# Performance work log

Measured on AMD Instinct MI355X. Metric: run time of the kernel, lower is better.

## Reference

```python
import jax, jax.numpy as jnp
import numpy as np

BN_EPS = 1e-5

def setup_inputs() -> dict:
    key = jax.random.key(0)
    ks = jax.random.split(key, 12)
    B = 32768
    x = jax.random.normal(ks[0], (B, 1, 28, 28), dtype=jnp.float32)
    conv_w = jax.random.normal(ks[1], (5, 1, 6, 6), dtype=jnp.float32) * 0.1
    conv_b = jax.random.normal(ks[2], (5,), dtype=jnp.float32) * 0.1
    bn2_gamma = jnp.ones((5,), jnp.float32) + jax.random.normal(ks[3], (5,), jnp.float32) * 0.05
    bn2_beta = jax.random.normal(ks[4], (5,), jnp.float32) * 0.05
    bn2_mean = jax.random.normal(ks[5], (5,), jnp.float32) * 0.1
    bn2_var = jax.random.uniform(ks[6], (5,), jnp.float32, 0.5, 1.5)
    fc_w = jax.random.normal(ks[7], (10, 125), dtype=jnp.float32) * 0.1
    fc_b = jax.random.normal(ks[8], (10,), dtype=jnp.float32) * 0.1
    bn1_gamma = jnp.ones((10,), jnp.float32) + jax.random.normal(ks[9], (10,), jnp.float32) * 0.05
    bn1_beta = jax.random.normal(ks[10], (10,), jnp.float32) * 0.05
    bn1_mean = jax.random.normal(ks[11], (10,), jnp.float32) * 0.1
    bn1_var = jnp.ones((10,), jnp.float32)
    return {"x": x, "conv_w": conv_w, "conv_b": conv_b,
            "bn2_gamma": bn2_gamma, "bn2_beta": bn2_beta, "bn2_mean": bn2_mean, "bn2_var": bn2_var,
            "fc_w": fc_w, "fc_b": fc_b,
            "bn1_gamma": bn1_gamma, "bn1_beta": bn1_beta, "bn1_mean": bn1_mean, "bn1_var": bn1_var}

def _sign(t):
    # torch Binarize = tensor.sign()
    return jnp.sign(t)

def reference(x, conv_w, conv_b, bn2_gamma, bn2_beta, bn2_mean, bn2_var,
              fc_w, fc_b, bn1_gamma, bn1_beta, bn1_mean, bn1_var):
    # BinarizeConv2d: binarize both input (C_in=1 != 3) and weight
    xb = _sign(x)
    wb = _sign(conv_w)
    y = jax.lax.conv_general_dilated(
        xb, wb, window_strides=(6, 6), padding=((2, 2), (2, 2)),
        dimension_numbers=("NCHW", "OIHW", "NCHW"))  # [B,5,5,5]
    y = y + conv_b[None, :, None, None]
    # BatchNorm2d (eval-mode running stats)
    y = (y - bn2_mean[None, :, None, None]) * (bn2_gamma / jnp.sqrt(bn2_var + BN_EPS))[None, :, None, None] + bn2_beta[None, :, None, None]
    # Hardtanh
    y = jnp.clip(y, -1.0, 1.0)
    # flatten to [B, 125]
    y = y.reshape(-1, 125)
    # BinarizeLinear: binarize input (125 != 784) and weight
    z = _sign(y) @ _sign(fc_w).T + fc_b
    # BatchNorm1d
    z = (z - bn1_mean) * (bn1_gamma / jnp.sqrt(bn1_var + BN_EPS)) + bn1_beta
    return jax.nn.log_softmax(z, axis=1)
```

## Files before the change

### kernel.cpp

```cpp
#include <hip/hip_runtime.h>
#include <cstdint>

#define BLK 256
#define SPB 8
#define RS  9
#define SS  (30*RS)
#define HDR 16
#define XS_INTS (HDR + SPB*SS)
#define YS_W 33

#if defined(__has_builtin)
# if __has_builtin(__builtin_amdgcn_sdot4)
#  define HAVE_SDOT4 1
# endif
#endif

__device__ __forceinline__ int dot4i8(int a, int b, int c) {
#ifdef HAVE_SDOT4
    return __builtin_amdgcn_sdot4(a, b, c, false);
#else
    int r = c;
    r += (((int)(a << 24)) >> 24) * (((int)(b << 24)) >> 24);
    r += (((int)(a << 16)) >> 24) * (((int)(b << 16)) >> 24);
    r += (((int)(a <<  8)) >> 24) * (((int)(b <<  8)) >> 24);
    r += (a >> 24) * (b >> 24);
    return r;
#endif
}

__device__ __forceinline__ int pack_sign4(float4 v) {
    int b0 = (v.x > 0.f) - (v.x < 0.f);
    int b1 = (v.y > 0.f) - (v.y < 0.f);
    int b2 = (v.z > 0.f) - (v.z < 0.f);
    int b3 = (v.w > 0.f) - (v.w < 0.f);
    return (b0 & 0xFF) | ((b1 & 0xFF) << 8) | ((b2 & 0xFF) << 16) | (b3 << 24);
}

__global__ void bnn_setup(const float* __restrict__ conv_w, const float* __restrict__ conv_b,
                          const float* __restrict__ bn2_g, const float* __restrict__ bn2_b,
                          const float* __restrict__ bn2_m, const float* __restrict__ bn2_v,
                          const float* __restrict__ fc_w,  const float* __restrict__ fc_b,
                          const float* __restrict__ bn1_g, const float* __restrict__ bn1_b,
                          const float* __restrict__ bn1_m, const float* __restrict__ bn1_v,
                          int* __restrict__ ws)
{
    const int tid = threadIdx.x;
    if (tid < 30) {
        int c = tid / 6, kr = tid - c * 6;
        const float* wp = conv_w + c * 36 + kr * 6;
        uint32_t a = 0, b = 0;
        #pragma unroll
        for (int k = 0; k < 4; k++) { int s = (wp[k]   > 0.f) - (wp[k]   < 0.f); a |= (uint32_t)(s & 0xFF) << (8 * k); }
        #pragma unroll
        for (int k = 0; k < 2; k++) { int s = (wp[4+k] > 0.f) - (wp[4+k] < 0.f); b |= (uint32_t)(s & 0xFF) << (8 * k); }
        ws[tid] = (int)a;
        ws[30 + tid] = (int)b;
    }
    for (int i = tid; i < 330; i += 64) {
        int o = i / 33, w = i - o * 33;
        uint32_t m = 0;
        #pragma unroll
        for (int k = 0; k < 4; k++) {
            int kk = w * 4 + k;
            if (kk < 125) { float f = fc_w[o * 125 + kk]; int s = (f > 0.f) - (f < 0.f); m |= (uint32_t)(s & 0xFF) << (8 * k); }
        }
        ws[60 + i] = (int)m;
    }
    if (tid < 5) {
        float sc = bn2_g[tid] / sqrtf(bn2_v[tid] + 1e-5f);
        ((float*)ws)[390 + tid] = sc;
        ((float*)ws)[395 + tid] = (conv_b[tid] - bn2_m[tid]) * sc + bn2_b[tid];
    }
    if (tid >= 32 && tid < 42) {
        int o = tid - 32;
        float sc = bn1_g[o] / sqrtf(bn1_v[o] + 1e-5f);
        ((float*)ws)[400 + o] = sc;
        ((float*)ws)[410 + o] = (fc_b[o] - bn1_m[o]) * sc + bn1_b[o];
    }
}

__global__ __launch_bounds__(BLK, 4)
void bnn_main(const float* __restrict__ x, const int* __restrict__ ws,
              float* __restrict__ out)
{
    __shared__ int   xsi[XS_INTS];
    __shared__ int   ysi[SPB * YS_W];
    __shared__ int   wsS[420];
    __shared__ float zf[SPB * 10];

    const int tid = threadIdx.x;
    const int blk = blockIdx.x;

    const float4* xg = (const float4*)x + (size_t)blk * (SPB * 196);
    float4 v[6]; float4 v6;
    #pragma unroll
    for (int k = 0; k < 6; k++) v[k] = xg[tid + k * BLK];
    const bool has7 = tid < (SPB * 196 - 6 * BLK);
    if (has7) v6 = xg[tid + 6 * BLK];

    for (int i = tid; i < 420; i += BLK) wsS[i] = ws[i];

    for (int i = tid; i < HDR + SPB * 74; i += BLK) {
        int idx;
        if (i < HDR) idx = i;
        else {
            int j = i - HDR, s = j / 74, k = j - s * 74;
            idx = HDR + s * SS + (k < 18 ? k : (2 + (k - 18) / 2) * RS + 7 + ((k - 18) & 1));
        }
        xsi[idx] = 0;
    }
    for (int i = tid; i < SPB * YS_W; i += BLK) ysi[i] = 0;

    #pragma unroll
    for (int k = 0; k < 6; k++) {
        int idx = tid + k * BLK;
        int s = idx / 196, rem = idx - s * 196;
        int r = rem / 7,   cq  = rem - r * 7;
        xsi[HDR + s * SS + (r + 2) * RS + cq] = pack_sign4(v[k]);
    }
    if (has7) {
        int idx = tid + 6 * BLK;
        int s = idx / 196, rem = idx - s * 196;
        int r = rem / 7,   cq  = rem - r * 7;
        xsi[HDR + s * SS + (r + 2) * RS + cq] = pack_sign4(v6);
    }
    __syncthreads();

    if (tid < 250) {
        const int c  = tid / 50;
        const int jb = tid - c * 50;
        int w0r[6], w1r[6];
        #pragma unroll
        for (int kr = 0; kr < 6; kr++) { w0r[kr] = wsS[c * 6 + kr]; w1r[kr] = wsS[30 + c * 6 + kr]; }
        const float sc = __int_as_float(wsS[390 + c]);
        const float bi = __int_as_float(wsS[395 + c]);
        #pragma unroll
        for (int t = 0; t < (SPB * 25) / 50; t++) {
            int j  = jb + 50 * t;
            int s  = j / 25, pos = j - s * 25;
            int oh = pos / 5, ow  = pos - oh * 5;
            int boff = 64 + s * (SS * 4) + oh * (6 * RS * 4) + ow * 6 - 2;
            int wi = boff >> 2;
            int sh = (boff & 3) * 8;
            int acc = 0;
            #pragma unroll
            for (int kr = 0; kr < 6; kr++) {
                uint32_t a0 = (uint32_t)xsi[wi + kr * RS];
                uint32_t a1 = (uint32_t)xsi[wi + kr * RS + 1];
                uint64_t vv = (((uint64_t)a1) << 32) | a0;
                vv >>= sh;
                acc = dot4i8((int)(uint32_t)vv,         w0r[kr], acc);
                acc = dot4i8((int)(uint32_t)(vv >> 32), w1r[kr], acc);
            }
            float yv = (float)acc * sc + bi;
            ((signed char*)ysi)[s * (YS_W * 4) + c * 25 + pos] =
                (signed char)((yv > 0.f) - (yv < 0.f));
        }
    }
    __syncthreads();

    if (tid < SPB * 10) {
        int s = tid / 10, o = tid - s * 10;
        int acc = 0;
        #pragma unroll
        for (int w = 0; w < 32; w++)
            acc = dot4i8(ysi[s * YS_W + w], wsS[60 + o * 33 + w], acc);
        zf[tid] = (float)acc * __int_as_float(wsS[400 + o]) + __int_as_float(wsS[410 + o]);
    }
    __syncthreads();

    if (tid < SPB) {
        float vv[10], mx = -1e30f;
        #pragma unroll
        for (int o = 0; o < 10; o++) { vv[o] = zf[tid * 10 + o]; mx = fmaxf(mx, vv[o]); }
        float l = 0.f;
        #pragma unroll
        for (int o = 0; o < 10; o++) l += __expf(vv[o] - mx);
        float lse = mx + __logf(l);
        #pragma unroll
        for (int o = 0; o < 10; o++) zf[tid * 10 + o] = vv[o] - lse;
    }
    __syncthreads();

    for (int i = tid; i < SPB * 10; i += BLK)
        out[(size_t)blk * (SPB * 10) + i] = zf[i];
}

extern "C" void kernel_launch(void* const* d_in, const int* in_sizes, int n_in,
                              void* d_out, int out_size, void* d_ws, size_t ws_size,
                              hipStream_t stream)
{
    const float* xp     = (const float*)d_in[0];
    const float* conv_w = (const float*)d_in[1];
    const float* conv_b = (const float*)d_in[2];
    const float* bn2_g  = (const float*)d_in[3];
    const float* bn2_b  = (const float*)d_in[4];
    const float* bn2_m  = (const float*)d_in[5];
    const float* bn2_v  = (const float*)d_in[6];
    const float* fc_w   = (const float*)d_in[7];
    const float* fc_b   = (const float*)d_in[8];
    const float* bn1_g  = (const float*)d_in[9];
    const float* bn1_b  = (const float*)d_in[10];
    const float* bn1_m  = (const float*)d_in[11];
    const float* bn1_v  = (const float*)d_in[12];
    float* outp = (float*)d_out;
    int*   ws   = (int*)d_ws;

    const int B = in_sizes[0] / 784;
    const int grid = B / SPB;

    bnn_setup<<<1, 64, 0, stream>>>(conv_w, conv_b, bn2_g, bn2_b, bn2_m, bn2_v,
                                    fc_w, fc_b, bn1_g, bn1_b, bn1_m, bn1_v, ws);
    bnn_main<<<grid, BLK, 0, stream>>>(xp, ws, outp);
}
```

Baseline: 179.8 us.

## Fuse weight setup into main kernel, double samples per block, restructure conv

Removes the separate setup kernel launch by having every block binarize conv/fc weights and fold the BN constants into shared memory. Doubles samples per block to 16 and rewrites the conv so each thread computes all 5 output channels for one spatial position. The 6x6 window is split into a 4-column part and a packed 2-column part, which cuts the dot-product count and reuses the loaded window across channels. In exchange every block redundantly reads and binarizes the small weight tensors, and register use rises from the 45 weight values held per thread.

```diff
diff --git a/kernel.cpp b/kernel.cpp
--- a/kernel.cpp
+++ b/kernel.cpp
@@ -2,12 +2,24 @@
 #include <cstdint>
 
 #define BLK 256
-#define SPB 8
+#define SPB 16
 #define RS  9
-#define SS  (30*RS)
+#define ROWS 30
+#define SS  (ROWS*RS)
 #define HDR 16
 #define XS_INTS (HDR + SPB*SS)
 #define YS_W 33
+#define NQ  ((SPB*196)/BLK)
+#define NREM (SPB*196 - NQ*BLK)
+
+#define W0_OFF  0
+#define W1P_OFF 30
+#define FC_OFF  45
+#define CSC_OFF 375
+#define CBI_OFF 380
+#define FSC_OFF 385
+#define FBI_OFF 395
+#define WS_TOT  405
 
 #if defined(__has_builtin)
 # if __has_builtin(__builtin_amdgcn_sdot4)
@@ -36,69 +48,72 @@
     return (b0 & 0xFF) | ((b1 & 0xFF) << 8) | ((b2 & 0xFF) << 16) | (b3 << 24);
 }
 
-__global__ void bnn_setup(const float* __restrict__ conv_w, const float* __restrict__ conv_b,
-                          const float* __restrict__ bn2_g, const float* __restrict__ bn2_b,
-                          const float* __restrict__ bn2_m, const float* __restrict__ bn2_v,
-                          const float* __restrict__ fc_w,  const float* __restrict__ fc_b,
-                          const float* __restrict__ bn1_g, const float* __restrict__ bn1_b,
-                          const float* __restrict__ bn1_m, const float* __restrict__ bn1_v,
-                          int* __restrict__ ws)
+__device__ __forceinline__ int sign8(float f) {
+    return (f > 0.f) - (f < 0.f);
+}
+
+__global__ __launch_bounds__(BLK, 4)
+void bnn_fused(const float* __restrict__ x,
+               const float* __restrict__ conv_w, const float* __restrict__ conv_b,
+               const float* __restrict__ bn2_g,  const float* __restrict__ bn2_b,
+               const float* __restrict__ bn2_m,  const float* __restrict__ bn2_v,
+               const float* __restrict__ fc_w,   const float* __restrict__ fc_b,
+               const float* __restrict__ bn1_g,  const float* __restrict__ bn1_b,
+               const float* __restrict__ bn1_m,  const float* __restrict__ bn1_v,
+               float* __restrict__ out)
 {
+    __shared__ int   xsi[XS_INTS];
+    __shared__ int   ysi[SPB * YS_W];
+    __shared__ int   wsS[WS_TOT];
+    __shared__ float zf[SPB * 10];
+
     const int tid = threadIdx.x;
+    const int blk = blockIdx.x;
+
+    const float4* xg = (const float4*)x + (size_t)blk * (SPB * 196);
+    float4 v[NQ]; float4 vr;
+    #pragma unroll
+    for (int k = 0; k < NQ; k++) v[k] = xg[tid + k * BLK];
+    const bool has = tid < NREM;
+    if (has) vr = xg[tid + NQ * BLK];
+
     if (tid < 30) {
         int c = tid / 6, kr = tid - c * 6;
         const float* wp = conv_w + c * 36 + kr * 6;
-        uint32_t a = 0, b = 0;
-        #pragma unroll
-        for (int k = 0; k < 4; k++) { int s = (wp[k]   > 0.f) - (wp[k]   < 0.f); a |= (uint32_t)(s & 0xFF) << (8 * k); }
-        #pragma unroll
-        for (int k = 0; k < 2; k++) { int s = (wp[4+k] > 0.f) - (wp[4+k] < 0.f); b |= (uint32_t)(s & 0xFF) << (8 * k); }
-        ws[tid] = (int)a;
-        ws[30 + tid] = (int)b;
-    }
-    for (int i = tid; i < 330; i += 64) {
+        uint32_t a = 0;
+        #pragma unroll
+        for (int k = 0; k < 4; k++) a |= (uint32_t)(sign8(wp[k]) & 0xFF) << (8 * k);
+        wsS[W0_OFF + tid] = (int)a;
+    } else if (tid >= 32 && tid < 47) {
+        int i = tid - 32, c = i / 3, p = i - c * 3;
+        const float* wp = conv_w + c * 36;
+        uint32_t a = 0;
+        a |= (uint32_t)(sign8(wp[(2*p)*6 + 4]) & 0xFF);
+        a |= (uint32_t)(sign8(wp[(2*p)*6 + 5]) & 0xFF) << 8;
+        a |= (uint32_t)(sign8(wp[(2*p+1)*6 + 4]) & 0xFF) << 16;
+        a |= (uint32_t)(sign8(wp[(2*p+1)*6 + 5]) & 0xFF) << 24;
+        wsS[W1P_OFF + i] = (int)a;
+    } else if (tid >= 48 && tid < 53) {
+        int c = tid - 48;
+        float sc = bn2_g[c] / sqrtf(bn2_v[c] + 1e-5f);
+        wsS[CSC_OFF + c] = __float_as_int(sc);
+        wsS[CBI_OFF + c] = __float_as_int((conv_b[c] - bn2_m[c]) * sc + bn2_b[c]);
+    } else if (tid >= 64 && tid < 74) {
+        int o = tid - 64;
+        float sc = bn1_g[o] / sqrtf(bn1_v[o] + 1e-5f);
+        wsS[FSC_OFF + o] = __float_as_int(sc);
+        wsS[FBI_OFF + o] = __float_as_int((fc_b[o] - bn1_m[o]) * sc + bn1_b[o]);
+    }
+    for (int i = tid; i < 330; i += BLK) {
         int o = i / 33, w = i - o * 33;
         uint32_t m = 0;
         #pragma unroll
         for (int k = 0; k < 4; k++) {
             int kk = w * 4 + k;
-            if (kk < 125) { float f = fc_w[o * 125 + kk]; int s = (f > 0.f) - (f < 0.f); m |= (uint32_t)(s & 0xFF) << (8 * k); }
-        }
-        ws[60 + i] = (int)m;
-    }
-    if (tid < 5) {
-        float sc = bn2_g[tid] / sqrtf(bn2_v[tid] + 1e-5f);
-        ((float*)ws)[390 + tid] = sc;
-        ((float*)ws)[395 + tid] = (conv_b[tid] - bn2_m[tid]) * sc + bn2_b[tid];
-    }
-    if (tid >= 32 && tid < 42) {
-        int o = tid - 32;
-        float sc = bn1_g[o] / sqrtf(bn1_v[o] + 1e-5f);
-        ((float*)ws)[400 + o] = sc;
-        ((float*)ws)[410 + o] = (fc_b[o] - bn1_m[o]) * sc + bn1_b[o];
-    }
-}
-
-__global__ __launch_bounds__(BLK, 4)
-void bnn_main(const float* __restrict__ x, const int* __restrict__ ws,
-              float* __restrict__ out)
-{
-    __shared__ int   xsi[XS_INTS];
-    __shared__ int   ysi[SPB * YS_W];
-    __shared__ int   wsS[420];
-    __shared__ float zf[SPB * 10];
-
-    const int tid = threadIdx.x;
-    const int blk = blockIdx.x;
-
-    const float4* xg = (const float4*)x + (size_t)blk * (SPB * 196);
-    float4 v[6]; float4 v6;
-    #pragma unroll
-    for (int k = 0; k < 6; k++) v[k] = xg[tid + k * BLK];
-    const bool has7 = tid < (SPB * 196 - 6 * BLK);
-    if (has7) v6 = xg[tid + 6 * BLK];
-
-    for (int i = tid; i < 420; i += BLK) wsS[i] = ws[i];
+            if (kk < 125) m |= (uint32_t)(sign8(fc_w[o * 125 + kk]) & 0xFF) << (8 * k);
+        }
+        wsS[FC_OFF + i] = (int)m;
+    }
 
     for (int i = tid; i < HDR + SPB * 74; i += BLK) {
         int idx;
@@ -112,49 +127,63 @@
     for (int i = tid; i < SPB * YS_W; i += BLK) ysi[i] = 0;
 
     #pragma unroll
-    for (int k = 0; k < 6; k++) {
+    for (int k = 0; k < NQ; k++) {
         int idx = tid + k * BLK;
         int s = idx / 196, rem = idx - s * 196;
         int r = rem / 7,   cq  = rem - r * 7;
         xsi[HDR + s * SS + (r + 2) * RS + cq] = pack_sign4(v[k]);
     }
-    if (has7) {
-        int idx = tid + 6 * BLK;
+    if (has) {
+        int idx = tid + NQ * BLK;
         int s = idx / 196, rem = idx - s * 196;
         int r = rem / 7,   cq  = rem - r * 7;
-        xsi[HDR + s * SS + (r + 2) * RS + cq] = pack_sign4(v6);
-    }
-    __syncthreads();
-
-    if (tid < 250) {
-        const int c  = tid / 50;
-        const int jb = tid - c * 50;
-        int w0r[6], w1r[6];
-        #pragma unroll
-        for (int kr = 0; kr < 6; kr++) { w0r[kr] = wsS[c * 6 + kr]; w1r[kr] = wsS[30 + c * 6 + kr]; }
-        const float sc = __int_as_float(wsS[390 + c]);
-        const float bi = __int_as_float(wsS[395 + c]);
-        #pragma unroll
-        for (int t = 0; t < (SPB * 25) / 50; t++) {
-            int j  = jb + 50 * t;
-            int s  = j / 25, pos = j - s * 25;
-            int oh = pos / 5, ow  = pos - oh * 5;
-            int boff = 64 + s * (SS * 4) + oh * (6 * RS * 4) + ow * 6 - 2;
-            int wi = boff >> 2;
-            int sh = (boff & 3) * 8;
-            int acc = 0;
-            #pragma unroll
-            for (int kr = 0; kr < 6; kr++) {
-                uint32_t a0 = (uint32_t)xsi[wi + kr * RS];
-                uint32_t a1 = (uint32_t)xsi[wi + kr * RS + 1];
-                uint64_t vv = (((uint64_t)a1) << 32) | a0;
-                vv >>= sh;
-                acc = dot4i8((int)(uint32_t)vv,         w0r[kr], acc);
-                acc = dot4i8((int)(uint32_t)(vv >> 32), w1r[kr], acc);
+        xsi[HDR + s * SS + (r + 2) * RS + cq] = pack_sign4(vr);
+    }
+    __syncthreads();
+
+    {
+        int w0[30], w1p[15]; float csc[5], cbi[5];
+        #pragma unroll
+        for (int i = 0; i < 30; i++) w0[i]  = wsS[W0_OFF + i];
+        #pragma unroll
+        for (int i = 0; i < 15; i++) w1p[i] = wsS[W1P_OFF + i];
+        #pragma unroll
+        for (int c = 0; c < 5; c++) {
+            csc[c] = __int_as_float(wsS[CSC_OFF + c]);
+            cbi[c] = __int_as_float(wsS[CBI_OFF + c]);
+        }
+        #pragma unroll
+        for (int it = 0; it < 2; it++) {
+            int j = tid + it * BLK;
+            if (j < SPB * 25) {
+                int s  = j / 25, pos = j - s * 25;
+                int oh = pos / 5, ow  = pos - oh * 5;
+                int q  = (6 * ow + 2) / 4 - 1;
+                int sh = ((6 * ow + 2) & 3) * 8;
+                int wi0 = HDR + s * SS + 54 * oh + q;
+                uint32_t e0[6], e1[6];
+                #pragma unroll
+                for (int kr = 0; kr < 6; kr++) {
+                    uint32_t a0 = (uint32_t)xsi[wi0 + 9 * kr];
+                    uint32_t a1 = (uint32_t)xsi[wi0 + 9 * kr + 1];
+                    uint64_t vv = ((((uint64_t)a1) << 32) | a0) >> sh;
+                    e0[kr] = (uint32_t)vv;
+                    e1[kr] = (uint32_t)(vv >> 32) & 0xFFFFu;
+                }
+                uint32_t e1p[3];
+                #pragma unroll
+                for (int p = 0; p < 3; p++) e1p[p] = e1[2*p] | (e1[2*p+1] << 16);
+                #pragma unroll
+                for (int c = 0; c < 5; c++) {
+                    int acc = 0;
+                    #pragma unroll
+                    for (int kr = 0; kr < 6; kr++) acc = dot4i8((int)e0[kr], w0[c*6+kr], acc);
+                    #pragma unroll
+                    for (int p = 0; p < 3; p++)    acc = dot4i8((int)e1p[p], w1p[c*3+p], acc);
+                    float yv = (float)acc * csc[c] + cbi[c];
+                    ((signed char*)ysi)[s * (YS_W*4) + c * 25 + pos] = (signed char)sign8(yv);
+                }
             }
-            float yv = (float)acc * sc + bi;
-            ((signed char*)ysi)[s * (YS_W * 4) + c * 25 + pos] =
-                (signed char)((yv > 0.f) - (yv < 0.f));
         }
     }
     __syncthreads();
@@ -164,8 +193,9 @@
         int acc = 0;
         #pragma unroll
         for (int w = 0; w < 32; w++)
-            acc = dot4i8(ysi[s * YS_W + w], wsS[60 + o * 33 + w], acc);
-        zf[tid] = (float)acc * __int_as_float(wsS[400 + o]) + __int_as_float(wsS[410 + o]);
+            acc = dot4i8(ysi[s * YS_W + w], wsS[FC_OFF + o * 33 + w], acc);
+        zf[tid] = (float)acc * __int_as_float(wsS[FSC_OFF + o])
+                             + __int_as_float(wsS[FBI_OFF + o]);
     }
     __syncthreads();
 
@@ -204,12 +234,11 @@
     const float* bn1_m  = (const float*)d_in[11];
     const float* bn1_v  = (const float*)d_in[12];
     float* outp = (float*)d_out;
-    int*   ws   = (int*)d_ws;
 
     const int B = in_sizes[0] / 784;
     const int grid = B / SPB;
-
-    bnn_setup<<<1, 64, 0, stream>>>(conv_w, conv_b, bn2_g, bn2_b, bn2_m, bn2_v,
-                                    fc_w, fc_b, bn1_g, bn1_b, bn1_m, bn1_v, ws);
-    bnn_main<<<grid, BLK, 0, stream>>>(xp, ws, outp);
-}
+    bnn_fused<<<grid, BLK, 0, stream>>>(xp, conv_w, conv_b,
+                                        bn2_g, bn2_b, bn2_m, bn2_v,
+                                        fc_w, fc_b, bn1_g, bn1_b, bn1_m, bn1_v,
+                                        outp);
+}
```

Result: no change. 179.7 us (-0.0%).
